# Optimization experiments

Measured on AMD Instinct MI355X. Metric: run time of the kernel, lower is better.

Reference implementation:

```python
import jax, jax.numpy as jnp
import numpy as np

N_NODES = 50000
N_EDGES = 800000
IN_DIM = 256
NHID = 64
OUT_DIM = 64
DEPTH = 4
P = 2.0


def _gcn_conv(x, W, b, src, dst, n):
    # PyG GCNConv: xW, add self-loops, sym-normalize, aggregate src->dst, + bias
    xw = x @ W
    loop = jnp.arange(n)
    s = jnp.concatenate([src, loop])
    d = jnp.concatenate([dst, loop])
    deg = jax.ops.segment_sum(jnp.ones_like(d, dtype=xw.dtype), d, num_segments=n)
    dis = jnp.where(deg > 0, jax.lax.rsqrt(jnp.maximum(deg, 1.0)), 0.0)
    w = dis[s] * dis[d]  # [E+n]
    out = jax.ops.segment_sum(w[:, None] * xw[s], d, num_segments=n)
    return out + b


def _g2_gate(x, W, b, src, dst, n):
    xg = jax.nn.relu(_gcn_conv(x, W, b, src, dst, n))
    diff = jnp.abs(xg[src] - xg[dst]) ** P  # [E, nhid]
    sums = jax.ops.segment_sum(diff, src, num_segments=n)
    cnt = jax.ops.segment_sum(jnp.ones((src.shape[0],), dtype=x.dtype), src, num_segments=n)
    return jnp.tanh(sums / jnp.maximum(cnt, 1.0)[:, None])


def setup_inputs() -> dict:
    key = jax.random.key(0)
    ks = jax.random.split(key, 10)
    x = jax.random.normal(ks[0], (N_NODES, IN_DIM), dtype=jnp.float32)
    edge_index = jax.random.randint(ks[1], (2, N_EDGES), 0, N_NODES, dtype=jnp.int64 if jax.config.jax_enable_x64 else jnp.int32)
    s = 0.05
    return {
        "x": x,
        "edge_index": edge_index,
        "enc_w": jax.random.normal(ks[2], (IN_DIM, NHID), dtype=jnp.float32) * s,
        "enc_b": jnp.zeros((NHID,), dtype=jnp.float32),
        "conv_w": jax.random.normal(ks[3], (NHID, NHID), dtype=jnp.float32) * s,
        "conv_b": jnp.zeros((NHID,), dtype=jnp.float32),
        "gg_w": jax.random.normal(ks[4], (NHID, NHID), dtype=jnp.float32) * s,
        "gg_b": jnp.zeros((NHID,), dtype=jnp.float32),
        "dec_w": jax.random.normal(ks[5], (NHID, OUT_DIM), dtype=jnp.float32) * s,
        "dec_b": jnp.zeros((OUT_DIM,), dtype=jnp.float32),
    }


def reference(x, edge_index, enc_w, enc_b, conv_w, conv_b, gg_w, gg_b, dec_w, dec_b):
    n = x.shape[0]
    src, dst = edge_index[0], edge_index[1]
    # eval mode: dropouts are identity
    X = jax.nn.relu(x @ enc_w + enc_b)
    for _ in range(DEPTH):
        X_ = jax.nn.relu(_gcn_conv(X, conv_w, conv_b, src, dst, n))
        tau = _g2_gate(X, gg_w, gg_b, src, dst, n)
        X = (1.0 - tau) * X + tau * X_
    X = jax.nn.relu(X @ dec_w + dec_b)
    return X
```

## Files before the change

kernel.cpp:

```cpp
#include <hip/hip_runtime.h>
#include <math.h>

#define NN 50000
#define NE 800000
#define IND 256
#define NH 64
#define DEPTH 4
#define PART_DIV 6250
#define SB 49


__device__ __forceinline__ unsigned short f2bf(float f) {
    unsigned int x = __float_as_uint(f);
    unsigned int r = (x + 0x7fffu + ((x >> 16) & 1u)) >> 16;
    return (unsigned short)r;
}
__device__ __forceinline__ unsigned int pack2bf(float lo, float hi) {
    return (unsigned int)f2bf(lo) | ((unsigned int)f2bf(hi) << 16);
}
__device__ __forceinline__ ushort4 f4_to_us4(float4 f) {
    ushort4 u;
    u.x = f2bf(f.x); u.y = f2bf(f.y); u.z = f2bf(f.z); u.w = f2bf(f.w);
    return u;
}
__device__ __forceinline__ void acc8(float* a, uint4 r) {
    a[0] += __uint_as_float(r.x << 16); a[1] += __uint_as_float(r.x & 0xffff0000u);
    a[2] += __uint_as_float(r.y << 16); a[3] += __uint_as_float(r.y & 0xffff0000u);
    a[4] += __uint_as_float(r.z << 16); a[5] += __uint_as_float(r.z & 0xffff0000u);
    a[6] += __uint_as_float(r.w << 16); a[7] += __uint_as_float(r.w & 0xffff0000u);
}
__device__ __forceinline__ void unpack8(float* a, uint4 r) {
    a[0] = __uint_as_float(r.x << 16); a[1] = __uint_as_float(r.x & 0xffff0000u);
    a[2] = __uint_as_float(r.y << 16); a[3] = __uint_as_float(r.y & 0xffff0000u);
    a[4] = __uint_as_float(r.z << 16); a[5] = __uint_as_float(r.z & 0xffff0000u);
    a[6] = __uint_as_float(r.w << 16); a[7] = __uint_as_float(r.w & 0xffff0000u);
}
__device__ __forceinline__ void accd8(float* a, const float* xg, uint4 r) {
    float e;
    e = xg[0] - __uint_as_float(r.x << 16);         a[0] += e * e;
    e = xg[1] - __uint_as_float(r.x & 0xffff0000u); a[1] += e * e;
    e = xg[2] - __uint_as_float(r.y << 16);         a[2] += e * e;
    e = xg[3] - __uint_as_float(r.y & 0xffff0000u); a[3] += e * e;
    e = xg[4] - __uint_as_float(r.z << 16);         a[4] += e * e;
    e = xg[5] - __uint_as_float(r.z & 0xffff0000u); a[5] += e * e;
    e = xg[6] - __uint_as_float(r.w << 16);         a[6] += e * e;
    e = xg[7] - __uint_as_float(r.w & 0xffff0000u); a[7] += e * e;
}
__device__ __forceinline__ float tanh_pos(float x) {
    float t = __expf(-2.f * x);
    return (1.f - t) / (1.f + t);
}


__global__ void count_deg_part(const int* __restrict__ src, const int* __restrict__ dst,
                               int* __restrict__ degin, int* __restrict__ degout,
                               int nGroups) {
    int p = blockIdx.x & 7;
    int g = blockIdx.x >> 3;
    for (int e = g * 256 + threadIdx.x; e < NE; e += nGroups * 256) {
        int s = src[e], d = dst[e];
        if (d / PART_DIV == p) atomicAdd(&degin[d], 1);
        if (s / PART_DIV == p) atomicAdd(&degout[s], 1);
    }
}

__global__ __launch_bounds__(512) void scan_p1(const int* __restrict__ in0,
                                               const int* __restrict__ in1,
                                               int* __restrict__ tmp,
                                               int* __restrict__ bsum) {
    int a = blockIdx.x / SB;
    int b = blockIdx.x % SB;
    const int* in = a ? in1 : in0;
    int t = threadIdx.x;
    int base = b * 1024 + t * 2;
    int v0 = (base < NN) ? in[base] : 0;
    int v1 = (base + 1 < NN) ? in[base + 1] : 0;
    int v = v0 + v1;
    int x = v;
#pragma unroll
    for (int off = 1; off < 64; off <<= 1) {
        int u = __shfl_up(x, off);
        if ((t & 63) >= off) x += u;
    }
    __shared__ int ws[8];
    int wid = t >> 6, lane = t & 63;
    if (lane == 63) ws[wid] = x;
    __syncthreads();
    if (t == 0) {
        int run = 0;
#pragma unroll
        for (int w = 0; w < 8; ++w) { int s = ws[w]; ws[w] = run; run += s; }
    }
    __syncthreads();
    x += ws[wid];
    int excl = x - v;
    if (base < NN) tmp[a * NN + base] = excl;
    if (base + 1 < NN) tmp[a * NN + base + 1] = excl + v0;
    if (t == 511) bsum[a * SB + b] = x;
}

__global__ __launch_bounds__(128) void scan_p2(int* __restrict__ bsum,
                                               int* __restrict__ out0,
                                               int* __restrict__ out1) {
    int t = threadIdx.x;
    int a = t >> 6, lane = t & 63;
    int v = (lane < SB) ? bsum[a * SB + lane] : 0;
    int x = v;
#pragma unroll
    for (int off = 1; off < 64; off <<= 1) {
        int u = __shfl_up(x, off);
        if (lane >= off) x += u;
    }
    if (lane < SB) bsum[a * SB + lane] = x - v;
    if (lane == SB - 1) {
        if (a == 0) out0[NN] = x; else out1[NN] = x;
    }
}

__global__ __launch_bounds__(512) void scan_p3(const int* __restrict__ tmp,
                                               const int* __restrict__ bsum,
                                               int* __restrict__ out0,
                                               int* __restrict__ out1) {
    int a = blockIdx.x / SB;
    int b = blockIdx.x % SB;
    int* out = a ? out1 : out0;
    int add = bsum[a * SB + b];
    int t = threadIdx.x;
    int base = b * 1024 + t * 2;
    if (base < NN) out[base] = tmp[a * NN + base] + add;
    if (base + 1 < NN) out[base + 1] = tmp[a * NN + base + 1] + add;
}

__global__ void init_node(const int* __restrict__ degin, const int* __restrict__ degout,
                          const int* __restrict__ off_dst, const int* __restrict__ off_src,
                          int* __restrict__ cur_dst, int* __restrict__ cur_src,
                          float* __restrict__ dis, float* __restrict__ cntf) {
    int i = blockIdx.x * blockDim.x + threadIdx.x;
    if (i < NN) {
        dis[i] = rsqrtf((float)(degin[i] + 1));
        int od = degout[i];
        cntf[i] = (float)(od > 0 ? od : 1);
        cur_dst[i] = off_dst[i];
        cur_src[i] = off_src[i];
    }
}

__global__ void fill_csr_part(const int* __restrict__ src, const int* __restrict__ dst,
                              int* __restrict__ cur_dst, int* __restrict__ cur_src,
                              int* __restrict__ srcs_by_dst, int* __restrict__ dsts_by_src,
                              int nGroups) {
    int p = blockIdx.x & 7;
    int g = blockIdx.x >> 3;
    for (int e = g * 256 + threadIdx.x; e < NE; e += nGroups * 256) {
        int s = src[e], d = dst[e];
        if (d / PART_DIV == p) {
            int pos = atomicAdd(&cur_dst[d], 1);
            srcs_by_dst[pos] = s;
        }
        if (s / PART_DIV == p) {
            int pos = atomicAdd(&cur_src[s], 1);
            dsts_by_src[pos] = d;
        }
    }
}

template<int K, bool RELU, bool WSC>
__global__ __launch_bounds__(256) void gemm64b(const float* __restrict__ X,
                                               const float* __restrict__ W,
                                               const float* __restrict__ bias,
                                               const float* __restrict__ rowscale,
                                               float* __restrict__ out,
                                               unsigned short* __restrict__ xsc, int n) {
    __shared__ float Ws[64 * 64];
    __shared__ float Xs[64][68];
    int tid = threadIdx.x;
    int row0 = blockIdx.x * 64;
    int r16 = tid >> 4;
    int cg = tid & 15;
    float4 acc[4];
#pragma unroll
    for (int t = 0; t < 4; ++t) acc[t] = make_float4(0.f, 0.f, 0.f, 0.f);

    for (int kc = 0; kc < K; kc += 64) {
        const float4* W4 = (const float4*)(W + (size_t)kc * 64);
        float4* Ws4 = (float4*)Ws;
#pragma unroll
        for (int t = 0; t < 4; ++t) Ws4[tid + t * 256] = W4[tid + t * 256];
#pragma unroll
        for (int t = 0; t < 4; ++t) {
            int r = r16 + t * 16;
            int grow = row0 + r;
            float4 xv = make_float4(0.f, 0.f, 0.f, 0.f);
            if (grow < n) xv = *(const float4*)(X + (size_t)grow * K + kc + cg * 4);
            Xs[r][cg * 4 + 0] = xv.x; Xs[r][cg * 4 + 1] = xv.y;
            Xs[r][cg * 4 + 2] = xv.z; Xs[r][cg * 4 + 3] = xv.w;
        }
        __syncthreads();
#pragma unroll
        for (int k = 0; k < 64; ++k) {
            float4 w4 = ((const float4*)Ws)[k * 16 + cg];
#pragma unroll
            for (int t = 0; t < 4; ++t) {
                float xv = Xs[r16 + t * 16][k];
                acc[t].x += xv * w4.x; acc[t].y += xv * w4.y;
                acc[t].z += xv * w4.z; acc[t].w += xv * w4.w;
            }
        }
        __syncthreads();
    }

    float4 b4 = ((const float4*)bias)[cg];
#pragma unroll
    for (int t = 0; t < 4; ++t) {
        int row = row0 + r16 + t * 16;
        if (row < n) {
            float4 o;
            o.x = acc[t].x + b4.x; o.y = acc[t].y + b4.y;
            o.z = acc[t].z + b4.z; o.w = acc[t].w + b4.w;
            if (RELU) {
                o.x = fmaxf(o.x, 0.f); o.y = fmaxf(o.y, 0.f);
                o.z = fmaxf(o.z, 0.f); o.w = fmaxf(o.w, 0.f);
            }
            ((float4*)(out + (size_t)row * 64))[cg] = o;
            if (WSC) {
                float s = rowscale[row];
                float4 o2 = make_float4(o.x * s, o.y * s, o.z * s, o.w * s);
                ((ushort4*)(xsc + (size_t)row * 64))[cg] = f4_to_us4(o2);
            }
        }
    }
}

template<bool OUTBF>
__global__ __launch_bounds__(256) void gemm64z(const float* __restrict__ Z,
                                               const float* __restrict__ W,
                                               const float* __restrict__ bias,
                                               float* __restrict__ outf,
                                               unsigned short* __restrict__ outb, int n) {
    __shared__ float Ws[64 * 64];
    __shared__ float Xs[64][68];
    int tid = threadIdx.x;
    int row0 = blockIdx.x * 64;
    int r16 = tid >> 4;
    int cg = tid & 15;
    float4 acc[4];
#pragma unroll
    for (int t = 0; t < 4; ++t) acc[t] = make_float4(0.f, 0.f, 0.f, 0.f);

    {
        const float4* W4 = (const float4*)W;
        float4* Ws4 = (float4*)Ws;
#pragma unroll
        for (int t = 0; t < 4; ++t) Ws4[tid + t * 256] = W4[tid + t * 256];
#pragma unroll
        for (int t = 0; t < 4; ++t) {
            int r = r16 + t * 16;
            int grow = row0 + t * 16 + r16;
            (void)grow;
            int gr = row0 + r;
            float4 xv = make_float4(0.f, 0.f, 0.f, 0.f);
            if (gr < n) xv = *(const float4*)(Z + (size_t)gr * 64 + cg * 4);
            Xs[r][cg * 4 + 0] = xv.x; Xs[r][cg * 4 + 1] = xv.y;
            Xs[r][cg * 4 + 2] = xv.z; Xs[r][cg * 4 + 3] = xv.w;
        }
        __syncthreads();
#pragma unroll
        for (int k = 0; k < 64; ++k) {
            float4 w4 = ((const float4*)Ws)[k * 16 + cg];
#pragma unroll
            for (int t = 0; t < 4; ++t) {
                float xv = Xs[r16 + t * 16][k];
                acc[t].x += xv * w4.x; acc[t].y += xv * w4.y;
                acc[t].z += xv * w4.z; acc[t].w += xv * w4.w;
            }
        }
    }

    float4 b4 = ((const float4*)bias)[cg];
#pragma unroll
    for (int t = 0; t < 4; ++t) {
        int row = row0 + r16 + t * 16;
        if (row < n) {
            float4 o;
            o.x = fmaxf(acc[t].x + b4.x, 0.f); o.y = fmaxf(acc[t].y + b4.y, 0.f);
            o.z = fmaxf(acc[t].z + b4.z, 0.f); o.w = fmaxf(acc[t].w + b4.w, 0.f);
            if (OUTBF) {
                ((ushort4*)(outb + (size_t)row * 64))[cg] = f4_to_us4(o);
            } else {
                ((float4*)(outf + (size_t)row * 64))[cg] = o;
            }
        }
    }
}

__global__ __launch_bounds__(256) void zgather(
    const unsigned short* __restrict__ Xbf,
    const int* __restrict__ off, const int* __restrict__ nbr,
    const float* __restrict__ dis, float* __restrict__ Z)
{
    int t = blockIdx.x * 256 + threadIdx.x;
    int node = t >> 3, l8 = t & 7;
    if (node >= NN) return;
    const uint4* Xb = (const uint4*)Xbf;
    float a[8];
    unpack8(a, Xb[(size_t)node * 8 + l8]);
    int lo = off[node], hi = off[node + 1];
    int j = lo;
    for (; j + 3 < hi; j += 4) {
        int s0 = nbr[j], s1 = nbr[j + 1], s2 = nbr[j + 2], s3 = nbr[j + 3];
        uint4 r0 = Xb[(size_t)s0 * 8 + l8];
        uint4 r1 = Xb[(size_t)s1 * 8 + l8];
        uint4 r2 = Xb[(size_t)s2 * 8 + l8];
        uint4 r3 = Xb[(size_t)s3 * 8 + l8];
        acc8(a, r0); acc8(a, r1); acc8(a, r2); acc8(a, r3);
    }
    for (; j < hi; ++j) {
        acc8(a, Xb[(size_t)nbr[j] * 8 + l8]);
    }
    float di = dis[node];
    float* zp = Z + (size_t)node * 64 + l8 * 8;
    *(float4*)(zp)     = make_float4(di * a[0], di * a[1], di * a[2], di * a[3]);
    *(float4*)(zp + 4) = make_float4(di * a[4], di * a[5], di * a[6], di * a[7]);
}

__global__ __launch_bounds__(256) void gate_update8(
    const unsigned short* __restrict__ Cbf, const float* __restrict__ Xn,
    float* __restrict__ X, unsigned short* __restrict__ Xbf,
    const int* __restrict__ off, const int* __restrict__ nbr,
    const float* __restrict__ cntf, const float* __restrict__ dis)
{
    int t = blockIdx.x * 256 + threadIdx.x;
    int node = t >> 3, l8 = t & 7;
    if (node >= NN) return;
    const uint4* Cb = (const uint4*)Cbf;
    float xg[8];
    unpack8(xg, Cb[(size_t)node * 8 + l8]);
    float a[8] = {0.f, 0.f, 0.f, 0.f, 0.f, 0.f, 0.f, 0.f};
    int lo = off[node], hi = off[node + 1];
    int j = lo;
    for (; j + 3 < hi; j += 4) {
        int d0 = nbr[j], d1 = nbr[j + 1], d2 = nbr[j + 2], d3 = nbr[j + 3];
        uint4 r0 = Cb[(size_t)d0 * 8 + l8];
        uint4 r1 = Cb[(size_t)d1 * 8 + l8];
        uint4 r2 = Cb[(size_t)d2 * 8 + l8];
        uint4 r3 = Cb[(size_t)d3 * 8 + l8];
        accd8(a, xg, r0); accd8(a, xg, r1); accd8(a, xg, r2); accd8(a, xg, r3);
    }
    for (; j < hi; ++j) {
        accd8(a, xg, Cb[(size_t)nbr[j] * 8 + l8]);
    }
    float inv = 1.f / cntf[node];
    float di = dis[node];
    const float* xop = X + (size_t)node * 64 + l8 * 8;
    const float* xnp = Xn + (size_t)node * 64 + l8 * 8;
    float o[8];
#pragma unroll
    for (int k = 0; k < 8; ++k) {
        float tau = tanh_pos(a[k] * inv);
        float xo = xop[k], xn = xnp[k];
        o[k] = xo + tau * (xn - xo);
    }
    float* xp = X + (size_t)node * 64 + l8 * 8;
    *(float4*)(xp)     = make_float4(o[0], o[1], o[2], o[3]);
    *(float4*)(xp + 4) = make_float4(o[4], o[5], o[6], o[7]);
    uint4 pk;
    pk.x = pack2bf(o[0] * di, o[1] * di);
    pk.y = pack2bf(o[2] * di, o[3] * di);
    pk.z = pack2bf(o[4] * di, o[5] * di);
    pk.w = pack2bf(o[6] * di, o[7] * di);
    ((uint4*)Xbf)[(size_t)node * 8 + l8] = pk;
}


extern "C" void kernel_launch(void* const* d_in, const int* in_sizes, int n_in,
                              void* d_out, int out_size, void* d_ws, size_t ws_size,
                              hipStream_t stream) {
    const float* x      = (const float*)d_in[0];
    const int*   ei     = (const int*)d_in[1];
    const float* enc_w  = (const float*)d_in[2];
    const float* enc_b  = (const float*)d_in[3];
    const float* conv_w = (const float*)d_in[4];
    const float* conv_b = (const float*)d_in[5];
    const float* gg_w   = (const float*)d_in[6];
    const float* gg_b   = (const float*)d_in[7];
    const float* dec_w  = (const float*)d_in[8];
    const float* dec_b  = (const float*)d_in[9];
    float* out = (float*)d_out;

    const int* src = ei;
    const int* dst = ei + NE;

    char* p = (char*)d_ws;
    auto alloc = [&](size_t bytes) -> void* {
        void* r = (void*)p;
        p += (bytes + 255) & ~(size_t)255;
        return r;
    };
    float* X   = (float*)alloc((size_t)NN * 64 * 4);
    float* Zb  = (float*)alloc((size_t)NN * 64 * 4);
    float* B   = (float*)alloc((size_t)NN * 64 * 4);
    unsigned short* Xbf = (unsigned short*)alloc((size_t)NN * 64 * 2);
    unsigned short* Cbf = (unsigned short*)alloc((size_t)NN * 64 * 2);
    float* dis  = (float*)alloc((size_t)NN * 4);
    float* cntf = (float*)alloc((size_t)NN * 4);
    int* degin   = (int*)alloc((size_t)NN * 4);
    int* degout  = (int*)alloc((size_t)NN * 4);
    int* off_dst = (int*)alloc((size_t)(NN + 1) * 4);
    int* off_src = (int*)alloc((size_t)(NN + 1) * 4);
    int* cur_dst = (int*)alloc((size_t)NN * 4);
    int* cur_src = (int*)alloc((size_t)NN * 4);
    int* sbd     = (int*)alloc((size_t)NE * 4);
    int* dbs     = (int*)alloc((size_t)NE * 4);
    int* stmp    = (int*)alloc((size_t)2 * NN * 4);
    int* bsum    = (int*)alloc((size_t)2 * SB * 4);

    hipMemsetAsync(degin, 0, (size_t)NN * 4, stream);
    hipMemsetAsync(degout, 0, (size_t)NN * 4, stream);

    const int NB = (NN + 255) / 256;
    const int NGROUPS = 104;
    count_deg_part<<<8 * NGROUPS, 256, 0, stream>>>(src, dst, degin, degout, NGROUPS);
    scan_p1<<<2 * SB, 512, 0, stream>>>(degin, degout, stmp, bsum);
    scan_p2<<<1, 128, 0, stream>>>(bsum, off_dst, off_src);
    scan_p3<<<2 * SB, 512, 0, stream>>>(stmp, bsum, off_dst, off_src);
    init_node<<<NB, 256, 0, stream>>>(degin, degout, off_dst, off_src,
                                      cur_dst, cur_src, dis, cntf);
    fill_csr_part<<<8 * NGROUPS, 256, 0, stream>>>(src, dst, cur_dst, cur_src,
                                                   sbd, dbs, NGROUPS);

    const int GB = (NN + 63) / 64;
    const int OB = ((NN * 8) + 255) / 256;

    gemm64b<IND, true, true><<<GB, 256, 0, stream>>>(x, enc_w, enc_b, dis, X, Xbf, NN);

    for (int l = 0; l < DEPTH; ++l) {
        zgather<<<OB, 256, 0, stream>>>(Xbf, off_dst, sbd, dis, Zb);
        gemm64z<false><<<GB, 256, 0, stream>>>(Zb, conv_w, conv_b, B, nullptr, NN);
        gemm64z<true><<<GB, 256, 0, stream>>>(Zb, gg_w, gg_b, nullptr, Cbf, NN);
        gate_update8<<<OB, 256, 0, stream>>>(Cbf, B, X, Xbf, off_src, dbs, cntf, dis);
    }

    gemm64b<NH, true, false><<<GB, 256, 0, stream>>>(X, dec_w, dec_b, nullptr, out, nullptr, NN);
}
```

Baseline: 697.1 us.

## Record per-edge atomic ranks during degree count; fill CSR without atomics

The degree-count kernel now runs one thread per edge and stores the value returned by each atomicAdd as the edge's rank within its destination and source buckets. The CSR fill then writes each edge at offset plus rank instead of doing a second round of atomics on cursor arrays, and the cursor initialisation is removed. The count kernel drops the partitioned scheme, so unpartitioned atomics may contend more, and two extra edge-sized rank arrays are written and read back. Separately, the two neighbour gather loops gain an 8-way unrolled path to keep more loads in flight.

```diff
diff --git a/kernel.cpp b/kernel.cpp
--- a/kernel.cpp
+++ b/kernel.cpp
@@ -52,15 +52,14 @@
 }
 
 
-__global__ void count_deg_part(const int* __restrict__ src, const int* __restrict__ dst,
+__global__ void count_deg_rank(const int* __restrict__ src, const int* __restrict__ dst,
                                int* __restrict__ degin, int* __restrict__ degout,
-                               int nGroups) {
-    int p = blockIdx.x & 7;
-    int g = blockIdx.x >> 3;
-    for (int e = g * 256 + threadIdx.x; e < NE; e += nGroups * 256) {
+                               int* __restrict__ rank_in, int* __restrict__ rank_out) {
+    int e = blockIdx.x * blockDim.x + threadIdx.x;
+    if (e < NE) {
         int s = src[e], d = dst[e];
-        if (d / PART_DIV == p) atomicAdd(&degin[d], 1);
-        if (s / PART_DIV == p) atomicAdd(&degout[s], 1);
+        rank_in[e]  = atomicAdd(&degin[d], 1);
+        rank_out[e] = atomicAdd(&degout[s], 1);
     }
 }
 
@@ -132,35 +131,26 @@
 }
 
 __global__ void init_node(const int* __restrict__ degin, const int* __restrict__ degout,
-                          const int* __restrict__ off_dst, const int* __restrict__ off_src,
-                          int* __restrict__ cur_dst, int* __restrict__ cur_src,
                           float* __restrict__ dis, float* __restrict__ cntf) {
     int i = blockIdx.x * blockDim.x + threadIdx.x;
     if (i < NN) {
         dis[i] = rsqrtf((float)(degin[i] + 1));
         int od = degout[i];
         cntf[i] = (float)(od > 0 ? od : 1);
-        cur_dst[i] = off_dst[i];
-        cur_src[i] = off_src[i];
     }
 }
 
 __global__ void fill_csr_part(const int* __restrict__ src, const int* __restrict__ dst,
-                              int* __restrict__ cur_dst, int* __restrict__ cur_src,
+                              const int* __restrict__ off_dst, const int* __restrict__ off_src,
+                              const int* __restrict__ rank_in, const int* __restrict__ rank_out,
                               int* __restrict__ srcs_by_dst, int* __restrict__ dsts_by_src,
                               int nGroups) {
     int p = blockIdx.x & 7;
     int g = blockIdx.x >> 3;
     for (int e = g * 256 + threadIdx.x; e < NE; e += nGroups * 256) {
         int s = src[e], d = dst[e];
-        if (d / PART_DIV == p) {
-            int pos = atomicAdd(&cur_dst[d], 1);
-            srcs_by_dst[pos] = s;
-        }
-        if (s / PART_DIV == p) {
-            int pos = atomicAdd(&cur_src[s], 1);
-            dsts_by_src[pos] = d;
-        }
+        if (d / PART_DIV == p) srcs_by_dst[off_dst[d] + rank_in[e]] = s;
+        if (s / PART_DIV == p) dsts_by_src[off_src[s] + rank_out[e]] = d;
     }
 }
 
@@ -255,8 +245,6 @@
 #pragma unroll
         for (int t = 0; t < 4; ++t) {
             int r = r16 + t * 16;
-            int grow = row0 + t * 16 + r16;
-            (void)grow;
             int gr = row0 + r;
             float4 xv = make_float4(0.f, 0.f, 0.f, 0.f);
             if (gr < n) xv = *(const float4*)(Z + (size_t)gr * 64 + cg * 4);
@@ -306,6 +294,20 @@
     unpack8(a, Xb[(size_t)node * 8 + l8]);
     int lo = off[node], hi = off[node + 1];
     int j = lo;
+    for (; j + 7 < hi; j += 8) {
+        int s0 = nbr[j],     s1 = nbr[j + 1], s2 = nbr[j + 2], s3 = nbr[j + 3];
+        int s4 = nbr[j + 4], s5 = nbr[j + 5], s6 = nbr[j + 6], s7 = nbr[j + 7];
+        uint4 r0 = Xb[(size_t)s0 * 8 + l8];
+        uint4 r1 = Xb[(size_t)s1 * 8 + l8];
+        uint4 r2 = Xb[(size_t)s2 * 8 + l8];
+        uint4 r3 = Xb[(size_t)s3 * 8 + l8];
+        uint4 r4 = Xb[(size_t)s4 * 8 + l8];
+        uint4 r5 = Xb[(size_t)s5 * 8 + l8];
+        uint4 r6 = Xb[(size_t)s6 * 8 + l8];
+        uint4 r7 = Xb[(size_t)s7 * 8 + l8];
+        acc8(a, r0); acc8(a, r1); acc8(a, r2); acc8(a, r3);
+        acc8(a, r4); acc8(a, r5); acc8(a, r6); acc8(a, r7);
+    }
     for (; j + 3 < hi; j += 4) {
         int s0 = nbr[j], s1 = nbr[j + 1], s2 = nbr[j + 2], s3 = nbr[j + 3];
         uint4 r0 = Xb[(size_t)s0 * 8 + l8];
@@ -338,6 +340,20 @@
     float a[8] = {0.f, 0.f, 0.f, 0.f, 0.f, 0.f, 0.f, 0.f};
     int lo = off[node], hi = off[node + 1];
     int j = lo;
+    for (; j + 7 < hi; j += 8) {
+        int d0 = nbr[j],     d1 = nbr[j + 1], d2 = nbr[j + 2], d3 = nbr[j + 3];
+        int d4 = nbr[j + 4], d5 = nbr[j + 5], d6 = nbr[j + 6], d7 = nbr[j + 7];
+        uint4 r0 = Cb[(size_t)d0 * 8 + l8];
+        uint4 r1 = Cb[(size_t)d1 * 8 + l8];
+        uint4 r2 = Cb[(size_t)d2 * 8 + l8];
+        uint4 r3 = Cb[(size_t)d3 * 8 + l8];
+        uint4 r4 = Cb[(size_t)d4 * 8 + l8];
+        uint4 r5 = Cb[(size_t)d5 * 8 + l8];
+        uint4 r6 = Cb[(size_t)d6 * 8 + l8];
+        uint4 r7 = Cb[(size_t)d7 * 8 + l8];
+        accd8(a, xg, r0); accd8(a, xg, r1); accd8(a, xg, r2); accd8(a, xg, r3);
+        accd8(a, xg, r4); accd8(a, xg, r5); accd8(a, xg, r6); accd8(a, xg, r7);
+    }
     for (; j + 3 < hi; j += 4) {
         int d0 = nbr[j], d1 = nbr[j + 1], d2 = nbr[j + 2], d3 = nbr[j + 3];
         uint4 r0 = Cb[(size_t)d0 * 8 + l8];
@@ -407,8 +423,8 @@
     int* degout  = (int*)alloc((size_t)NN * 4);
     int* off_dst = (int*)alloc((size_t)(NN + 1) * 4);
     int* off_src = (int*)alloc((size_t)(NN + 1) * 4);
-    int* cur_dst = (int*)alloc((size_t)NN * 4);
-    int* cur_src = (int*)alloc((size_t)NN * 4);
+    int* rank_in  = (int*)alloc((size_t)NE * 4);
+    int* rank_out = (int*)alloc((size_t)NE * 4);
     int* sbd     = (int*)alloc((size_t)NE * 4);
     int* dbs     = (int*)alloc((size_t)NE * 4);
     int* stmp    = (int*)alloc((size_t)2 * NN * 4);
@@ -417,16 +433,16 @@
     hipMemsetAsync(degin, 0, (size_t)NN * 4, stream);
     hipMemsetAsync(degout, 0, (size_t)NN * 4, stream);
 
+    const int EB = (NE + 255) / 256;
     const int NB = (NN + 255) / 256;
     const int NGROUPS = 104;
-    count_deg_part<<<8 * NGROUPS, 256, 0, stream>>>(src, dst, degin, degout, NGROUPS);
+    count_deg_rank<<<EB, 256, 0, stream>>>(src, dst, degin, degout, rank_in, rank_out);
     scan_p1<<<2 * SB, 512, 0, stream>>>(degin, degout, stmp, bsum);
     scan_p2<<<1, 128, 0, stream>>>(bsum, off_dst, off_src);
     scan_p3<<<2 * SB, 512, 0, stream>>>(stmp, bsum, off_dst, off_src);
-    init_node<<<NB, 256, 0, stream>>>(degin, degout, off_dst, off_src,
-                                      cur_dst, cur_src, dis, cntf);
-    fill_csr_part<<<8 * NGROUPS, 256, 0, stream>>>(src, dst, cur_dst, cur_src,
-                                                   sbd, dbs, NGROUPS);
+    init_node<<<NB, 256, 0, stream>>>(degin, degout, dis, cntf);
+    fill_csr_part<<<8 * NGROUPS, 256, 0, stream>>>(src, dst, off_dst, off_src,
+                                                   rank_in, rank_out, sbd, dbs, NGROUPS);
 
     const int GB = (NN + 63) / 64;
     const int OB = ((NN * 8) + 255) / 256;
```

Result: faster. 680.1 us (-2.4%).
